# Optimization experiments

Hardware: AMD Instinct MI355X
Metric: run time of the kernel (lower is better)

The kernel has to match this reference:

```python
import math
import jax, jax.numpy as jnp
import numpy as np

V, D, H, L, F, S, B = 32000, 768, 12, 6, 3072, 2048, 4
DK = D // H


def setup_inputs() -> dict:
    key = jax.random.key(0)
    ks = jax.random.split(key, 16)
    sc = 0.02
    n = jax.random.normal
    inp = {
        "input_ids": jax.random.randint(ks[0], (B, S), 0, V, dtype=jnp.int64)
        if jax.config.jax_enable_x64 else jax.random.randint(ks[0], (B, S), 0, V, dtype=jnp.int32),
        "emb": n(ks[1], (V, D), jnp.float32) * sc,
        "Wq": n(ks[2], (L, D, D), jnp.float32) * sc, "bq": jnp.zeros((L, D), jnp.float32),
        "Wk": n(ks[3], (L, D, D), jnp.float32) * sc, "bk": jnp.zeros((L, D), jnp.float32),
        "Wv": n(ks[4], (L, D, D), jnp.float32) * sc, "bv": jnp.zeros((L, D), jnp.float32),
        "Wo": n(ks[5], (L, D, D), jnp.float32) * sc, "bo": jnp.zeros((L, D), jnp.float32),
        "W1": n(ks[6], (L, D, F), jnp.float32) * sc, "b1": jnp.zeros((L, F), jnp.float32),
        "W2": n(ks[7], (L, F, D), jnp.float32) * sc, "b2": jnp.zeros((L, D), jnp.float32),
        "gamma": jnp.ones((L, D), jnp.float32), "beta": jnp.zeros((L, D), jnp.float32),
    }
    return inp


def _pos_encoding(seq_len, d):
    pos = jnp.arange(seq_len, dtype=jnp.float32)[:, None]                  # [S,1]
    div = jnp.exp(jnp.arange(0, d, 2, dtype=jnp.float32) * (-math.log(10000.0) / d))
    ang = pos * div                                                        # [S,D/2]
    return jnp.stack([jnp.sin(ang), jnp.cos(ang)], axis=-1).reshape(seq_len, d)


def _layernorm(x, g, b, eps=1e-5):
    mu = x.mean(-1, keepdims=True)
    var = ((x - mu) ** 2).mean(-1, keepdims=True)
    return (x - mu) * jax.lax.rsqrt(var + eps) * g + b


def _forward(input_ids, emb, Wq, bq, Wk, bk, Wv, bv, Wo, bo, W1, b1, W2, b2, gamma, beta):
    mask = (input_ids != 1)[:, None, None, :]                              # [B,1,1,S]
    x = emb[input_ids] + _pos_encoding(input_ids.shape[1], emb.shape[1])   # [B,S,D]

    def layer(x, p):
        wq, bq_, wk, bk_, wv, bv_, wo, bo_, w1, b1_, w2, b2_, g, bt = p
        def heads(h):  # [B,S,D] -> [B,H,S,DK]
            return h.reshape(B, S, H, DK).transpose(0, 2, 1, 3)
        q = heads(x @ wq + bq_)
        k = heads(x @ wk + bk_)
        v = heads(x @ wv + bv_)
        scores = jnp.einsum("bhqd,bhkd->bhqk", q, k) / math.sqrt(DK)
        scores = jnp.where(mask, scores, -1e9)
        attn = jax.nn.softmax(scores, axis=-1)
        o = jnp.einsum("bhqk,bhkd->bhqd", attn, v)
        o = o.transpose(0, 2, 1, 3).reshape(B, S, D) @ wo + bo_
        x1 = _layernorm(x + o, g, bt)
        ff = jax.nn.relu(x1 @ w1 + b1_) @ w2 + b2_
        return _layernorm(x1 + ff, g, bt), None  # same norm params reused (as in source)

    x, _ = jax.lax.scan(layer, x, (Wq, bq, Wk, bk, Wv, bv, Wo, bo, W1, b1, W2, b2, gamma, beta))
    return x.mean(axis=1)                                                  # [B,D]


def reference(input_ids, emb, Wq, bq, Wk, bk, Wv, bv, Wo, bo, W1, b1, W2, b2, gamma, beta):
    return _forward(input_ids, emb, Wq, bq, Wk, bk, Wv, bv, Wo, bo, W1, b1, W2, b2, gamma, beta)
```

## Files before the change

### kernel.cpp

```cpp
#include <hip/hip_runtime.h>
#include <hip/hip_bf16.h>
#include <math.h>

typedef unsigned short u16;
typedef unsigned long long u64;
using bf16x8 = __attribute__((ext_vector_type(8))) short;
using f32x4  = __attribute__((ext_vector_type(4))) float;

static constexpr int kD = 768;
static constexpr int kH = 12;
static constexpr int kL = 6;
static constexpr int kF = 3072;
static constexpr int kS = 2048;
static constexpr int kB = 4;
static constexpr int kQW = 2304;
static constexpr int kNT = kB * kS;

static constexpr float kQScale = 0.18033688011112043f;

__device__ __forceinline__ u16 f2bf(float f) {
    return __bfloat16_as_ushort(__float2bfloat16(f));
}
__device__ __forceinline__ float b2f(u16 u) {
    return __uint_as_float((unsigned)u << 16);
}
__device__ __forceinline__ unsigned cvtpk(float a, float b) {
    unsigned d;
    asm volatile("v_cvt_pk_bf16_f32 %0, %1, %2" : "=v"(d) : "v"(a), "v"(b));
    return d;
}
__device__ __forceinline__ float exp2fast(float x) {
#if __has_builtin(__builtin_amdgcn_exp2f)
    return __builtin_amdgcn_exp2f(x);
#else
    return __expf(x * 0.6931471805599453f);
#endif
}

__device__ __forceinline__ void gload16(const void* g, void* l) {
    auto gp = reinterpret_cast<const __attribute__((address_space(1))) unsigned int*>(
        reinterpret_cast<uintptr_t>(g));
    auto lp = reinterpret_cast<__attribute__((address_space(3))) unsigned int*>(
        reinterpret_cast<uintptr_t>(l));
    __builtin_amdgcn_global_load_lds(gp, lp, 16, 0, 0);
}

__global__ __launch_bounds__(256) void embed_pe(
    const int* __restrict__ ids, const float* __restrict__ emb,
    u16* __restrict__ xbf)
{
    const int t = blockIdx.x;
    const int s = t & (kS - 1);
    const int id = ids[t];
#pragma unroll
    for (int j = 0; j < 3; ++j) {
        const int d = threadIdx.x + (j << 8);
        const float i2 = (float)((d >> 1) << 1);
        const float dv = __expf(i2 * (-9.210340371976184f / 768.f));
        const float ang = (float)s * dv;
        const float pe = (d & 1) ? cosf(ang) : sinf(ang);
        xbf[(size_t)t * kD + d] = f2bf(emb[(size_t)id * kD + d] + pe);
    }
}

__global__ __launch_bounds__(256) void embed_pe_f32(
    const int* __restrict__ ids, const float* __restrict__ emb,
    float* __restrict__ x)
{
    const int t = blockIdx.x;
    const int s = t & (kS - 1);
    const int id = ids[t];
#pragma unroll
    for (int j = 0; j < 3; ++j) {
        const int d = threadIdx.x + (j << 8);
        const float i2 = (float)((d >> 1) << 1);
        const float dv = __expf(i2 * (-9.210340371976184f / 768.f));
        const float ang = (float)s * dv;
        const float pe = (d & 1) ? cosf(ang) : sinf(ang);
        x[(size_t)t * kD + d] = emb[(size_t)id * kD + d] + pe;
    }
}

__global__ __launch_bounds__(64) void mk_maskbits(const int* __restrict__ ids,
                                                  u64* __restrict__ mbits)
{
    const int w = blockIdx.x;
    const int lane = threadIdx.x;
    const u64 m = __ballot(ids[(size_t)w * 64 + lane] != 1);
    if (lane == 0) mbits[w] = m;
}

__global__ __launch_bounds__(256) void bias_build(
    const float* __restrict__ bq, const float* __restrict__ bk,
    const float* __restrict__ bv, const float* __restrict__ bo,
    const float* __restrict__ b1, const float* __restrict__ b2,
    float* __restrict__ ba)
{
    const int i = blockIdx.x * 256 + threadIdx.x;
    if (i >= 6 * 6912) return;
    const int l = i / 6912, p = i % 6912;
    float v;
    if      (p < 768)  v = bq[l * 768 + p] * kQScale;
    else if (p < 1536) v = bk[l * 768 + p - 768];
    else if (p < 2304) v = bv[l * 768 + p - 1536];
    else if (p < 3072) v = bo[l * 768 + p - 2304];
    else if (p < 6144) v = b1[(size_t)l * 3072 + p - 3072];
    else               v = b2[l * 768 + p - 6144];
    ba[i] = v;
}

static constexpr size_t OFF_WO = (size_t)2304 * 768;
static constexpr size_t OFF_W1 = OFF_WO + (size_t)768 * 768;
static constexpr size_t OFF_W2 = OFF_W1 + (size_t)3072 * 768;
static constexpr size_t WARENA_E = OFF_W2 + (size_t)768 * 3072;

__global__ __launch_bounds__(256) void cvt_all(
    const float* __restrict__ Wq, const float* __restrict__ Wk,
    const float* __restrict__ Wv, const float* __restrict__ Wo,
    const float* __restrict__ W1, const float* __restrict__ W2,
    u16* __restrict__ wa)
{
    __shared__ float T[64][68];
    const int t = blockIdx.x;
    const float* S; u16* Dp; int Nsrc, Kdst, srow0, scol0; float sc = 1.f;
    if (t < 432) {
        const int ni = t % 36, ki = t / 36;
        const int ng = ni * 64;
        const int sel = ng / 768;
        scol0 = ng % 768; srow0 = ki * 64;
        S = (sel == 0) ? Wq : (sel == 1) ? Wk : Wv;
        if (sel == 0) sc = kQScale;
        Nsrc = 768; Kdst = 768;
        Dp = wa + (size_t)ng * 768 + srow0;
    } else if (t < 576) {
        const int tt = t - 432; const int ni = tt % 12, ki = tt / 12;
        scol0 = ni * 64; srow0 = ki * 64;
        S = Wo; Nsrc = 768; Kdst = 768;
        Dp = wa + OFF_WO + (size_t)(ni * 64) * 768 + srow0;
    } else if (t < 1152) {
        const int tt = t - 576; const int ni = tt % 48, ki = tt / 48;
        scol0 = ni * 64; srow0 = ki * 64;
        S = W1; Nsrc = 3072; Kdst = 768;
        Dp = wa + OFF_W1 + (size_t)(ni * 64) * 768 + srow0;
    } else {
        const int tt = t - 1152; const int ni = tt % 12, ki = tt / 12;
        scol0 = ni * 64; srow0 = ki * 64;
        S = W2; Nsrc = 768; Kdst = 3072;
        Dp = wa + OFF_W2 + (size_t)(ni * 64) * 3072 + srow0;
    }
    const int tid = threadIdx.x;
#pragma unroll
    for (int i = 0; i < 4; ++i) {
        const int idx = tid + (i << 8);
        const int kr = idx >> 4;
        const int nc = (idx & 15) << 2;
        const float4 v = *(const float4*)(S + (size_t)(srow0 + kr) * Nsrc + scol0 + nc);
        T[kr][nc] = v.x; T[kr][nc + 1] = v.y; T[kr][nc + 2] = v.z; T[kr][nc + 3] = v.w;
    }
    __syncthreads();
#pragma unroll
    for (int i = 0; i < 4; ++i) {
        const int idx = tid + (i << 8);
        const int nr = idx >> 4;
        const int kc = (idx & 15) << 2;
        ushort4 o;
        o.x = f2bf(T[kc][nr] * sc);     o.y = f2bf(T[kc + 1][nr] * sc);
        o.z = f2bf(T[kc + 2][nr] * sc); o.w = f2bf(T[kc + 3][nr] * sc);
        *(ushort4*)(Dp + (size_t)nr * Kdst + kc) = o;
    }
}

__global__ __launch_bounds__(256) void gemm_bf16(
    const u16* __restrict__ A, const u16* __restrict__ Bt,
    const float* __restrict__ bias, void* __restrict__ Cv,
    u16* __restrict__ vTp, int M, int N, int K, int mode)
{
    __shared__ u16 As[2][4096];
    __shared__ u16 Bs[2][4096];
    const int tid = threadIdx.x;
    const int l = tid & 63;
    const int lo = l & 15, hi = l >> 4;
    const int w = tid >> 6, wr = w >> 1, wc = w & 1;

    int brow = blockIdx.x, bcol = blockIdx.y;
    const int gx = gridDim.x;
    if ((gx & 7) == 0) {
        const int id = blockIdx.y * gx + blockIdx.x;
        const int xcd = id & 7, idx = id >> 3;
        const int rpx = gx >> 3;
        brow = xcd * rpx + (idx % rpx);
        bcol = idx / rpx;
    }
    const size_t row0 = (size_t)brow * 128;
    const size_t col0 = (size_t)bcol * 128;

    const int c0 = tid, c1 = tid + 256;
    const int r0 = c0 >> 2, g0 = (c0 & 3) ^ ((r0 >> 1) & 3);
    const int r1 = c1 >> 2, g1 = (c1 & 3) ^ ((r1 >> 1) & 3);
    const u16* a0 = A  + (row0 + r0) * K + g0 * 8;
    const u16* a1 = A  + (row0 + r1) * K + g1 * 8;
    const u16* b0 = Bt + (col0 + r0) * K + g0 * 8;
    const u16* b1 = Bt + (col0 + r1) * K + g1 * 8;

    f32x4 acc[4][4];
#pragma unroll
    for (int i = 0; i < 4; ++i)
#pragma unroll
        for (int j = 0; j < 4; ++j)
#pragma unroll
            for (int r = 0; r < 4; ++r) acc[i][j][r] = 0.f;

    int aoff[4], boff[4];
#pragma unroll
    for (int i = 0; i < 4; ++i) {
        const int ra = wr * 64 + i * 16 + lo;
        aoff[i] = ra * 32 + ((hi ^ ((ra >> 1) & 3)) << 3);
        const int rb = wc * 64 + i * 16 + lo;
        boff[i] = rb * 32 + ((hi ^ ((rb >> 1) & 3)) << 3);
    }

    const int NT = K >> 5;
    gload16(a0, As[0] + c0 * 8);
    gload16(a1, As[0] + c1 * 8);
    gload16(b0, Bs[0] + c0 * 8);
    gload16(b1, Bs[0] + c1 * 8);

    int cur = 0;
    for (int t = 0; t < NT; ++t) {
        if (t + 1 < NT) {
            const int k0 = (t + 1) << 5;
            const int nb = cur ^ 1;
            gload16(a0 + k0, As[nb] + c0 * 8);
            gload16(a1 + k0, As[nb] + c1 * 8);
            gload16(b0 + k0, Bs[nb] + c0 * 8);
            gload16(b1 + k0, Bs[nb] + c1 * 8);
            asm volatile("s_waitcnt vmcnt(4)" ::: "memory");
        } else {
            asm volatile("s_waitcnt vmcnt(0)" ::: "memory");
        }
        __builtin_amdgcn_s_barrier();
        bf16x8 af[4], bfr[4];
#pragma unroll
        for (int i = 0; i < 4; ++i) af[i]  = *(const bf16x8*)&As[cur][aoff[i]];
#pragma unroll
        for (int j = 0; j < 4; ++j) bfr[j] = *(const bf16x8*)&Bs[cur][boff[j]];
#pragma unroll
        for (int i = 0; i < 4; ++i)
#pragma unroll
            for (int j = 0; j < 4; ++j)
                acc[i][j] = __builtin_amdgcn_mfma_f32_16x16x32_bf16(
                    af[i], bfr[j], acc[i][j], 0, 0, 0);
        asm volatile("s_waitcnt lgkmcnt(0)" ::: "memory");
        __builtin_amdgcn_sched_barrier(0);
        __builtin_amdgcn_s_barrier();
        cur ^= 1;
    }

    const bool vmode = (mode == 3) && (col0 >= 1536);
    if (vmode) {
#pragma unroll
        for (int i = 0; i < 4; ++i) {
            const size_t rbase = row0 + wr * 64 + i * 16 + hi * 4;
            const size_t tb = (rbase >> 6) * 64;
            const int k0 = (int)(rbase & 63);
            const int pos = (((k0 >> 2) & 3) << 3) + (((k0 >> 4) & 1) << 2)
                          + ((k0 >> 5) << 5);
#pragma unroll
            for (int j = 0; j < 4; ++j) {
                const size_t c = col0 + wc * 64 + j * 16 + lo;
                const float bs = bias[c];
                const size_t d = c - 1536;
                ushort4 o;
                o.x = f2bf(acc[i][j][0] + bs);
                o.y = f2bf(acc[i][j][1] + bs);
                o.z = f2bf(acc[i][j][2] + bs);
                o.w = f2bf(acc[i][j][3] + bs);
                *(ushort4*)(vTp + d * (size_t)M + tb + pos) = o;
            }
        }
        return;
    }

#pragma unroll
    for (int i = 0; i < 4; ++i) {
        const size_t rbase = row0 + wr * 64 + i * 16 + hi * 4;
#pragma unroll
        for (int j = 0; j < 4; ++j) {
            const size_t c = col0 + wc * 64 + j * 16 + lo;
            const float bs = bias[c];
#pragma unroll
            for (int r = 0; r < 4; ++r) {
                float v = acc[i][j][r] + bs;
                if (mode == 2) v = fmaxf(v, 0.f);
                ((u16*)Cv)[(rbase + r) * (size_t)N + c] = f2bf(v);
            }
        }
    }
}

__global__ __launch_bounds__(256) void attn_mfma(
    const u16* __restrict__ QKV, const u16* __restrict__ vT,
    const u64* __restrict__ mbits, u16* __restrict__ O)
{
    __shared__ u16 Ks[2][4096];
    __shared__ u16 Vs[2][4096];

    const int tid = threadIdx.x, l = tid & 63, w = tid >> 6;
    const int lo = l & 15, hi = l >> 4;
    const int h = blockIdx.y, b = blockIdx.z;
    const int q0 = blockIdx.x << 6;

    bf16x8 qf0, qf1;
    {
        const u16* qp = QKV + ((size_t)(b * kS + q0 + w * 16 + lo)) * kQW
                            + h * 64 + hi * 8;
        qf0 = *(const bf16x8*)qp;
        qf1 = *(const bf16x8*)(qp + 32);
    }

    const int ga = tid, gb = tid + 256;
    const int rwA = ga >> 3, sxA = ga & 7, EA = sxA ^ (rwA & 7);
    const int rwB = gb >> 3, sxB = gb & 7, EB = sxB ^ (rwB & 7);
    const u16* Kbase = QKV + (size_t)(b * kS) * kQW + 768 + h * 64;
    const u16* Vbase = vT + (size_t)(h * 64) * kNT + b * kS;

    f32x4 accO[4];
#pragma unroll
    for (int n = 0; n < 4; ++n)
#pragma unroll
        for (int r = 0; r < 4; ++r) accO[n][r] = 0.f;
    float m = -3.0e38f, lsum = 0.f;

    const int ksw = (lo & 7) << 3;
    constexpr int NTt = kS / 64;

    gload16(Kbase + (size_t)rwA * kQW + EA * 8, Ks[0] + ga * 8);
    gload16(Kbase + (size_t)rwB * kQW + EB * 8, Ks[0] + gb * 8);
    gload16(Vbase + (size_t)rwA * kNT + EA * 8, Vs[0] + ga * 8);
    gload16(Vbase + (size_t)rwB * kNT + EB * 8, Vs[0] + gb * 8);

    int cur = 0;
    for (int kt = 0; kt < NTt; ++kt) {
        asm volatile("s_waitcnt vmcnt(0)" ::: "memory");
        __syncthreads();

        if (kt + 1 < NTt) {
            const size_t kof = (size_t)((kt + 1) << 6) * kQW;
            const size_t vof = (size_t)((kt + 1) << 6);
            u16* kd = Ks[cur ^ 1];
            u16* vd = Vs[cur ^ 1];
            gload16(Kbase + kof + (size_t)rwA * kQW + EA * 8, kd + ga * 8);
            gload16(Kbase + kof + (size_t)rwB * kQW + EB * 8, kd + gb * 8);
            gload16(Vbase + (size_t)rwA * kNT + vof + EA * 8, vd + ga * 8);
            gload16(Vbase + (size_t)rwB * kNT + vof + EB * 8, vd + gb * 8);
        }

        f32x4 st[4];
        __builtin_amdgcn_s_setprio(1);
#pragma unroll
        for (int j = 0; j < 4; ++j) {
#pragma unroll
            for (int r = 0; r < 4; ++r) st[j][r] = 0.f;
            const int kb2 = (j * 16 + lo) * 64;
            const bf16x8 k0 = *(const bf16x8*)&Ks[cur][kb2 + ((hi * 8)      ^ ksw)];
            const bf16x8 k1 = *(const bf16x8*)&Ks[cur][kb2 + ((hi * 8 + 32) ^ ksw)];
            st[j] = __builtin_amdgcn_mfma_f32_16x16x32_bf16(k0, qf0, st[j], 0, 0, 0);
            st[j] = __builtin_amdgcn_mfma_f32_16x16x32_bf16(k1, qf1, st[j], 0, 0, 0);
        }
        __builtin_amdgcn_s_setprio(0);

        float rmax = st[0][0];
#pragma unroll
        for (int j = 0; j < 4; ++j)
#pragma unroll
            for (int r = 0; r < 4; ++r) rmax = fmaxf(rmax, st[j][r]);
        rmax = fmaxf(rmax, __shfl_xor(rmax, 16));
        rmax = fmaxf(rmax, __shfl_xor(rmax, 32));

        const bool skip = __all(rmax <= m + 11.0f);
        if (!skip) {
            const float mn = fmaxf(m, rmax);
            const float corr = exp2fast(m - mn);
            m = mn;
            lsum *= corr;
            float c2[4];
#pragma unroll
            for (int r = 0; r < 4; ++r) c2[r] = __shfl(corr, hi * 4 + r);
#pragma unroll
            for (int n = 0; n < 4; ++n)
#pragma unroll
                for (int r = 0; r < 4; ++r) accO[n][r] *= c2[r];
        }

#pragma unroll
        for (int j = 0; j < 4; ++j)
#pragma unroll
            for (int r = 0; r < 4; ++r) st[j][r] = exp2fast(st[j][r] - m);

        const u64 mb = mbits[b * 32 + kt];
        if (mb != ~0ull) {
#pragma unroll
            for (int j = 0; j < 4; ++j)
#pragma unroll
                for (int r = 0; r < 4; ++r)
                    if (!((mb >> (j * 16 + hi * 4 + r)) & 1)) st[j][r] = 0.f;
        }

        float ts = 0.f;
#pragma unroll
        for (int j = 0; j < 4; ++j)
#pragma unroll
            for (int r = 0; r < 4; ++r) ts += st[j][r];
        ts += __shfl_xor(ts, 16);
        ts += __shfl_xor(ts, 32);
        lsum += ts;

        union PU { unsigned u[4]; bf16x8 v; } p0, p1;
        p0.u[0] = cvtpk(st[0][0], st[0][1]); p0.u[1] = cvtpk(st[0][2], st[0][3]);
        p0.u[2] = cvtpk(st[1][0], st[1][1]); p0.u[3] = cvtpk(st[1][2], st[1][3]);
        p1.u[0] = cvtpk(st[2][0], st[2][1]); p1.u[1] = cvtpk(st[2][2], st[2][3]);
        p1.u[2] = cvtpk(st[3][0], st[3][1]); p1.u[3] = cvtpk(st[3][2], st[3][3]);

        __builtin_amdgcn_s_setprio(1);
#pragma unroll
        for (int n = 0; n < 4; ++n) {
            const int vb2 = (n * 16 + lo) * 64;
            const bf16x8 v0 = *(const bf16x8*)&Vs[cur][vb2 + ((hi * 8)      ^ ksw)];
            const bf16x8 v1 = *(const bf16x8*)&Vs[cur][vb2 + ((hi * 8 + 32) ^ ksw)];
            accO[n] = __builtin_amdgcn_mfma_f32_16x16x32_bf16(p0.v, v0, accO[n], 0, 0, 0);
            accO[n] = __builtin_amdgcn_mfma_f32_16x16x32_bf16(p1.v, v1, accO[n], 0, 0, 0);
        }
        __builtin_amdgcn_s_setprio(0);
        cur ^= 1;
    }

    float linv[4];
#pragma unroll
    for (int r = 0; r < 4; ++r) linv[r] = 1.f / __shfl(lsum, hi * 4 + r);
#pragma unroll
    for (int n = 0; n < 4; ++n)
#pragma unroll
        for (int r = 0; r < 4; ++r)
            O[((size_t)(b * kS + q0 + w * 16 + hi * 4 + r)) * kD
              + h * 64 + n * 16 + lo] = f2bf(accO[n][r] * linv[r]);
}

__global__ __launch_bounds__(256) void add_ln_bf(
    const u16* __restrict__ a, const u16* __restrict__ r,
    const float* __restrict__ g, const float* __restrict__ bt,
    u16* __restrict__ out)
{
    const int lane = threadIdx.x & 63;
    const size_t row = (size_t)blockIdx.x * 4 + (threadIdx.x >> 6);
    const ushort4* a4 = (const ushort4*)(a + row * kD);
    const ushort4* r4 = (const ushort4*)(r + row * kD);
    float v[3][4];
    float s = 0.f;
#pragma unroll
    for (int j = 0; j < 3; ++j) {
        const ushort4 av = a4[j * 64 + lane];
        const ushort4 rv = r4[j * 64 + lane];
        v[j][0] = b2f(av.x) + b2f(rv.x);
        v[j][1] = b2f(av.y) + b2f(rv.y);
        v[j][2] = b2f(av.z) + b2f(rv.z);
        v[j][3] = b2f(av.w) + b2f(rv.w);
        s += v[j][0] + v[j][1] + v[j][2] + v[j][3];
    }
#pragma unroll
    for (int off = 32; off; off >>= 1) s += __shfl_xor(s, off);
    const float mu = s * (1.f / 768.f);
    float vs = 0.f;
#pragma unroll
    for (int j = 0; j < 3; ++j)
#pragma unroll
        for (int e = 0; e < 4; ++e) {
            const float t0 = v[j][e] - mu;
            vs = fmaf(t0, t0, vs);
        }
#pragma unroll
    for (int off = 32; off; off >>= 1) vs += __shfl_xor(vs, off);
    const float rstd = rsqrtf(vs * (1.f / 768.f) + 1e-5f);
    const float4* g4 = (const float4*)g;
    const float4* b4 = (const float4*)bt;
#pragma unroll
    for (int j = 0; j < 3; ++j) {
        const float4 gv = g4[j * 64 + lane];
        const float4 bv = b4[j * 64 + lane];
        ushort4 o;
        o.x = f2bf((v[j][0] - mu) * rstd * gv.x + bv.x);
        o.y = f2bf((v[j][1] - mu) * rstd * gv.y + bv.y);
        o.z = f2bf((v[j][2] - mu) * rstd * gv.z + bv.z);
        o.w = f2bf((v[j][3] - mu) * rstd * gv.w + bv.w);
        ((ushort4*)(out + row * kD))[j * 64 + lane] = o;
    }
}

__global__ __launch_bounds__(192) void mean_part_bf(
    const u16* __restrict__ x, float* __restrict__ mred)
{
    const int c = blockIdx.x, b = blockIdx.y;
    const int d = threadIdx.x * 4;
    const u16* base = x + ((size_t)b * kS + c * 32) * kD + d;
    float s0 = 0.f, s1 = 0.f, s2 = 0.f, s3 = 0.f;
#pragma unroll 8
    for (int t = 0; t < 32; ++t) {
        const ushort4 u = *(const ushort4*)(base + (size_t)t * kD);
        s0 += b2f(u.x); s1 += b2f(u.y); s2 += b2f(u.z); s3 += b2f(u.w);
    }
    float4 o; o.x = s0; o.y = s1; o.z = s2; o.w = s3;
    *(float4*)(mred + ((size_t)b * 64 + c) * kD + d) = o;
}

__global__ __launch_bounds__(256) void mean_fin(
    const float* __restrict__ mred, float* __restrict__ out)
{
    const int d = blockIdx.x * 256 + threadIdx.x;
    const int b = blockIdx.y;
    float s = 0.f;
#pragma unroll
    for (int c = 0; c < 64; ++c) s += mred[((size_t)b * 64 + c) * kD + d];
    out[b * kD + d] = s * (1.f / 2048.f);
}

__global__ __launch_bounds__(256) void add_ln_f32(
    const float* __restrict__ a, const float* __restrict__ r,
    const float* __restrict__ g, const float* __restrict__ bt,
    float* __restrict__ out)
{
    const int lane = threadIdx.x & 63;
    const size_t row = (size_t)blockIdx.x * 4 + (threadIdx.x >> 6);
    const float4* a4 = (const float4*)(a + row * kD);
    const float4* r4 = (const float4*)(r + row * kD);
    float4 v[3];
    float s = 0.f;
#pragma unroll
    for (int j = 0; j < 3; ++j) {
        const float4 av = a4[j * 64 + lane];
        const float4 rv = r4[j * 64 + lane];
        v[j].x = av.x + rv.x; v[j].y = av.y + rv.y;
        v[j].z = av.z + rv.z; v[j].w = av.w + rv.w;
        s += v[j].x + v[j].y + v[j].z + v[j].w;
    }
#pragma unroll
    for (int off = 32; off; off >>= 1) s += __shfl_xor(s, off);
    const float mu = s * (1.f / 768.f);
    float vs = 0.f;
#pragma unroll
    for (int j = 0; j < 3; ++j) {
        float t0 = v[j].x - mu, t1 = v[j].y - mu, t2 = v[j].z - mu, t3 = v[j].w - mu;
        vs = fmaf(t0, t0, fmaf(t1, t1, fmaf(t2, t2, fmaf(t3, t3, vs))));
    }
#pragma unroll
    for (int off = 32; off; off >>= 1) vs += __shfl_xor(vs, off);
    const float rstd = rsqrtf(vs * (1.f / 768.f) + 1e-5f);
    const float4* g4 = (const float4*)g;
    const float4* b4 = (const float4*)bt;
#pragma unroll
    for (int j = 0; j < 3; ++j) {
        const float4 gv = g4[j * 64 + lane];
        const float4 bv = b4[j * 64 + lane];
        float4 o;
        o.x = (v[j].x - mu) * rstd * gv.x + bv.x;
        o.y = (v[j].y - mu) * rstd * gv.y + bv.y;
        o.z = (v[j].z - mu) * rstd * gv.z + bv.z;
        o.w = (v[j].w - mu) * rstd * gv.w + bv.w;
        ((float4*)(out + row * kD))[j * 64 + lane] = o;
    }
}

__global__ __launch_bounds__(256) void mean_s(
    const float* __restrict__ x, float* __restrict__ out)
{
    const int d = blockIdx.x * 256 + threadIdx.x;
    const int b = blockIdx.y;
    float s = 0.f;
    for (int t = 0; t < kS; ++t) s += x[((size_t)b * kS + t) * kD + d];
    out[b * kD + d] = s * (1.f / 2048.f);
}

__global__ __launch_bounds__(256) void gemm_f32(
    const float* __restrict__ A, const float* __restrict__ W,
    const float* __restrict__ bias, float* __restrict__ C,
    int M, int N, int K, int relu)
{
    __shared__ float As[16][68];
    __shared__ float Bs[16][68];
    const int tid = threadIdx.x;
    const int row0 = blockIdx.x << 6;
    const int col0 = blockIdx.y << 6;
    const int tx = tid & 15, ty = tid >> 4;
    const int ar = tid >> 2;
    const int ak = (tid & 3) << 2;
    const int bk = tid >> 4;
    const int bc = (tid & 15) << 2;
    float acc[4][4] = {};
    const float* Ap = A + (size_t)(row0 + ar) * K + ak;
    const float* Wp = W + (size_t)bk * N + col0 + bc;
    for (int k0 = 0; k0 < K; k0 += 16) {
        const float4 a4 = *(const float4*)(Ap + k0);
        const float4 b4 = *(const float4*)(Wp + (size_t)k0 * N);
        __syncthreads();
        As[ak + 0][ar] = a4.x; As[ak + 1][ar] = a4.y;
        As[ak + 2][ar] = a4.z; As[ak + 3][ar] = a4.w;
        *(float4*)&Bs[bk][bc] = b4;
        __syncthreads();
#pragma unroll
        for (int kk = 0; kk < 16; ++kk) {
            const float4 av = *(const float4*)&As[kk][ty << 2];
            const float4 bv = *(const float4*)&Bs[kk][tx << 2];
            const float aa[4] = {av.x, av.y, av.z, av.w};
            const float bb[4] = {bv.x, bv.y, bv.z, bv.w};
#pragma unroll
            for (int i = 0; i < 4; ++i)
#pragma unroll
                for (int j = 0; j < 4; ++j)
                    acc[i][j] = fmaf(aa[i], bb[j], acc[i][j]);
        }
    }
#pragma unroll
    for (int i = 0; i < 4; ++i) {
        const int row = row0 + (ty << 2) + i;
#pragma unroll
        for (int j = 0; j < 4; ++j) {
            const int col = col0 + (tx << 2) + j;
            float v = acc[i][j] + bias[col];
            if (relu) v = fmaxf(v, 0.f);
            C[(size_t)row * N + col] = v;
        }
    }
}

__global__ __launch_bounds__(256) void attn_fused(
    const float* __restrict__ Q, const float* __restrict__ Km,
    const float* __restrict__ Vm, const int* __restrict__ ids,
    float* __restrict__ O)
{
    __shared__ float Ksf[64 * 64];
    __shared__ float Vtf[64 * 64];
    __shared__ float Qs[16][64];
    __shared__ float Psf[4][4][64];
    const int tid = threadIdx.x;
    const int w = tid >> 6;
    const int lane = tid & 63;
    const int h = blockIdx.y, b = blockIdx.z;
    const int qrow0 = blockIdx.x << 4;
    {
        const int r = tid >> 4;
        const int c4 = tid & 15;
        const float4 q4 = *(const float4*)(
            Q + ((size_t)(b * kS + qrow0 + r)) * kD + h * 64 + (c4 << 2));
        Qs[r][(c4 << 2) + 0] = q4.x * 0.125f;
        Qs[r][(c4 << 2) + 1] = q4.y * 0.125f;
        Qs[r][(c4 << 2) + 2] = q4.z * 0.125f;
        Qs[r][(c4 << 2) + 3] = q4.w * 0.125f;
    }
    float m[4], lsum[4], o[4];
#pragma unroll
    for (int r = 0; r < 4; ++r) { m[r] = -3.0e38f; lsum[r] = 0.f; o[r] = 0.f; }
    for (int kt = 0; kt < kS / 64; ++kt) {
        __syncthreads();
#pragma unroll
        for (int i = 0; i < 4; ++i) {
            const int lin = tid + (i << 8);
            const int row = lin >> 4;
            const int s4 = lin & 15;
            const size_t gro = ((size_t)(b * kS + (kt << 6) + row)) * kD + h * 64 + (s4 << 2);
            const float4 k4 = *(const float4*)(Km + gro);
            ((float4*)Ksf)[(row << 4) + (s4 ^ (row & 7))] = k4;
            const float4 v4 = *(const float4*)(Vm + gro);
            const int ksl = row >> 2, ke = row & 3;
            const int d0 = s4 << 2;
            Vtf[(d0 + 0) * 64 + ((ksl ^ ((d0 + 0) & 7)) << 2) + ke] = v4.x;
            Vtf[(d0 + 1) * 64 + ((ksl ^ ((d0 + 1) & 7)) << 2) + ke] = v4.y;
            Vtf[(d0 + 2) * 64 + ((ksl ^ ((d0 + 2) & 7)) << 2) + ke] = v4.z;
            Vtf[(d0 + 3) * 64 + ((ksl ^ ((d0 + 3) & 7)) << 2) + ke] = v4.w;
        }
        __syncthreads();
        const bool masked = (ids[(size_t)b * kS + (kt << 6) + lane] == 1);
        float scr[4] = {0.f, 0.f, 0.f, 0.f};
#pragma unroll
        for (int i16 = 0; i16 < 16; ++i16) {
            const float4 kv = ((const float4*)Ksf)[(lane << 4) + (i16 ^ (lane & 7))];
#pragma unroll
            for (int r = 0; r < 4; ++r) {
                const float4 qv = *(const float4*)&Qs[(w << 2) + r][i16 << 2];
                scr[r] = fmaf(kv.x, qv.x, fmaf(kv.y, qv.y,
                          fmaf(kv.z, qv.z, fmaf(kv.w, qv.w, scr[r]))));
            }
        }
#pragma unroll
        for (int r = 0; r < 4; ++r) {
            float sm = masked ? -3.0e38f : scr[r];
#pragma unroll
            for (int off = 32; off; off >>= 1) sm = fmaxf(sm, __shfl_xor(sm, off));
            const float mn = fmaxf(m[r], sm);
            const float cr = __expf(m[r] - mn);
            const float pv = masked ? 0.f : __expf(scr[r] - mn);
            float ps = pv;
#pragma unroll
            for (int off = 32; off; off >>= 1) ps += __shfl_xor(ps, off);
            lsum[r] = lsum[r] * cr + ps;
            o[r] *= cr;
            m[r] = mn;
            Psf[w][r][lane] = pv;
        }
#pragma unroll
        for (int i16 = 0; i16 < 16; ++i16) {
            const float4 vv = ((const float4*)Vtf)[(lane << 4) + (i16 ^ (lane & 7))];
#pragma unroll
            for (int r = 0; r < 4; ++r) {
                const float4 pv = *(const float4*)&Psf[w][r][i16 << 2];
                o[r] = fmaf(pv.x, vv.x, fmaf(pv.y, vv.y,
                        fmaf(pv.z, vv.z, fmaf(pv.w, vv.w, o[r]))));
            }
        }
    }
#pragma unroll
    for (int r = 0; r < 4; ++r)
        O[((size_t)(b * kS + qrow0 + (w << 2) + r)) * kD + h * 64 + lane] =
            o[r] / lsum[r];
}

extern "C" void kernel_launch(void* const* d_in, const int* in_sizes, int n_in,
                              void* d_out, int out_size, void* d_ws, size_t ws_size,
                              hipStream_t stream)
{
    const int*   ids   = (const int*)  d_in[0];
    const float* emb   = (const float*)d_in[1];
    const float* Wq    = (const float*)d_in[2];
    const float* bq    = (const float*)d_in[3];
    const float* Wk    = (const float*)d_in[4];
    const float* bk    = (const float*)d_in[5];
    const float* Wv    = (const float*)d_in[6];
    const float* bv    = (const float*)d_in[7];
    const float* Wo    = (const float*)d_in[8];
    const float* bo    = (const float*)d_in[9];
    const float* W1    = (const float*)d_in[10];
    const float* b1    = (const float*)d_in[11];
    const float* W2    = (const float*)d_in[12];
    const float* b2    = (const float*)d_in[13];
    const float* gamma = (const float*)d_in[14];
    const float* beta  = (const float*)d_in[15];
    float* out = (float*)d_out;

    const size_t BUFE = (size_t)kB * kS * kD;
    const size_t WDD  = (size_t)kD * kD;
    const size_t WDF  = (size_t)kD * kF;
    const size_t HIDE = (size_t)kB * kS * kF;
    const int NTOK = kB * kS;

    const size_t NEED = BUFE * 2 * 4
                      + HIDE * 2
                      + WARENA_E * 2
                      + (size_t)6 * 6912 * 4
                      + 128 * 8
                      + (size_t)kB * 64 * kD * 4;

    if (ws_size >= NEED) {
        u16*   xb  = (u16*)d_ws;
        u16*   x1b = xb + BUFE;
        u16*   ao  = x1b + BUFE;
        u16*   ob  = ao + BUFE;
        u16*   sc  = ob + BUFE;
        u16*   vtb = sc + (size_t)NTOK * kQW;
        u16*   wa  = sc + HIDE;
        float* ba  = (float*)(wa + WARENA_E);
        u64*   mbt = (u64*)(ba + 6 * 6912);
        float* mrd = (float*)(mbt + 128);

        embed_pe<<<NTOK, 256, 0, stream>>>(ids, emb, xb);
        mk_maskbits<<<kB * kS / 64, 64, 0, stream>>>(ids, mbt);
        bias_build<<<(6 * 6912 + 255) / 256, 256, 0, stream>>>(
            bq, bk, bv, bo, b1, b2, ba);

        for (int l = 0; l < kL; ++l) {
            const size_t oDD = (size_t)l * WDD;
            const size_t oDF = (size_t)l * WDF;
            const float* bl = ba + (size_t)l * 6912;
            const float* gl  = gamma + (size_t)l * kD;
            const float* btl = beta  + (size_t)l * kD;

            cvt_all<<<1728, 256, 0, stream>>>(
                Wq + oDD, Wk + oDD, Wv + oDD, Wo + oDD, W1 + oDF, W2 + oDF, wa);

            gemm_bf16<<<dim3(64, 18), 256, 0, stream>>>(
                xb, wa, bl, sc, vtb, NTOK, kQW, kD, 3);

            attn_mfma<<<dim3(kS / 64, kH, kB), 256, 0, stream>>>(
                sc, vtb, mbt, ao);

            gemm_bf16<<<dim3(64, 6), 256, 0, stream>>>(
                ao, wa + OFF_WO, bl + 2304, ob, nullptr, NTOK, kD, kD, 1);

            add_ln_bf<<<NTOK / 4, 256, 0, stream>>>(xb, ob, gl, btl, x1b);

            gemm_bf16<<<dim3(64, 24), 256, 0, stream>>>(
                x1b, wa + OFF_W1, bl + 3072, sc, nullptr, NTOK, kF, kD, 2);
            gemm_bf16<<<dim3(64, 6), 256, 0, stream>>>(
                sc, wa + OFF_W2, bl + 6144, ob, nullptr, NTOK, kD, kF, 1);

            add_ln_bf<<<NTOK / 4, 256, 0, stream>>>(x1b, ob, gl, btl, xb);
        }

        mean_part_bf<<<dim3(64, kB), 192, 0, stream>>>(xb, mrd);
        mean_fin<<<dim3(kD / 256, kB), 256, 0, stream>>>(mrd, out);
        return;
    }

    if (ws_size < 5 * BUFE * sizeof(float)) return;
    float* xb = (float*)d_ws;
    float* kb = xb + BUFE;
    float* qb = kb + BUFE;
    float* vb = qb + BUFE;
    float* obf = vb + BUFE;
    float* hb = qb;

    embed_pe_f32<<<NTOK, 256, 0, stream>>>(ids, emb, xb);
    for (int l = 0; l < kL; ++l) {
        const size_t oDD = (size_t)l * WDD;
        const size_t oDF = (size_t)l * WDF;
        gemm_f32<<<dim3(NTOK / 64, kD / 64), 256, 0, stream>>>(
            xb, Wq + oDD, bq + (size_t)l * kD, qb, NTOK, kD, kD, 0);
        gemm_f32<<<dim3(NTOK / 64, kD / 64), 256, 0, stream>>>(
            xb, Wk + oDD, bk + (size_t)l * kD, kb, NTOK, kD, kD, 0);
        gemm_f32<<<dim3(NTOK / 64, kD / 64), 256, 0, stream>>>(
            xb, Wv + oDD, bv + (size_t)l * kD, vb, NTOK, kD, kD, 0);
        attn_fused<<<dim3(kS / 16, kH, kB), 256, 0, stream>>>(qb, kb, vb, ids, obf);
        gemm_f32<<<dim3(NTOK / 64, kD / 64), 256, 0, stream>>>(
            obf, Wo + oDD, bo + (size_t)l * kD, qb, NTOK, kD, kD, 0);
        add_ln_f32<<<NTOK / 4, 256, 0, stream>>>(xb, qb,
            gamma + (size_t)l * kD, beta + (size_t)l * kD, kb);
        for (int c = 0; c < 2; ++c) {
            const size_t ro = (size_t)c * 4096;
            gemm_f32<<<dim3(4096 / 64, kF / 64), 256, 0, stream>>>(
                kb + ro * kD, W1 + oDF, b1 + (size_t)l * kF, hb, 4096, kF, kD, 1);
            gemm_f32<<<dim3(4096 / 64, kD / 64), 256, 0, stream>>>(
                hb, W2 + oDF, b2 + (size_t)l * kD, obf + ro * kD, 4096, kD, kF, 0);
        }
        add_ln_f32<<<NTOK / 4, 256, 0, stream>>>(kb, obf,
            gamma + (size_t)l * kD, beta + (size_t)l * kD, xb);
    }
    mean_s<<<dim3(kD / 256, kB), 256, 0, stream>>>(xb, out);
}
```

Measured before the change: 1.662 ms.

## Add 256x256 triple-buffered GEMM and 128-query attention blocks with XCD remap

Adds a 512-thread GEMM kernel with 256x256 output tiles and a three-stage LDS pipeline, used for the QKV and FFN-up projections. Larger tiles raise data reuse per loaded byte, and the extra stage lets global loads run further ahead of the MFMA work. The attention kernel now runs 512 threads covering 128 queries per block, with a flattened block index remapped across the XCDs so each K/V tile is shared by more queries. Costs include much higher register and LDS use per block, fewer blocks in the grid (288 and 384) which may leave CUs idle, and the old V-transpose path is removed from the 128x128 GEMM.

```diff
diff --git a/kernel.cpp b/kernel.cpp
--- a/kernel.cpp
+++ b/kernel.cpp
@@ -170,6 +170,142 @@
     }
 }
 
+__global__ __launch_bounds__(512, 1) void gemm256(
+    const u16* __restrict__ A, const u16* __restrict__ Bt,
+    const float* __restrict__ bias, void* __restrict__ Cv,
+    u16* __restrict__ vTp, int M, int N, int K, int mode)
+{
+    __shared__ u16 As[3][8192];
+    __shared__ u16 Bs[3][8192];
+    const int tid = threadIdx.x;
+    const int l = tid & 63;
+    const int lo = l & 15, hi = l >> 4;
+    const int w = tid >> 6, wr = w >> 2, wc = w & 3;
+
+    int brow = blockIdx.x, bcol = blockIdx.y;
+    const int gx = gridDim.x;
+    if ((gx & 7) == 0) {
+        const int id = blockIdx.y * gx + blockIdx.x;
+        const int xcd = id & 7, idx = id >> 3;
+        const int rpx = gx >> 3;
+        brow = xcd * rpx + (idx % rpx);
+        bcol = idx / rpx;
+    }
+    const size_t row0 = (size_t)brow * 256;
+    const size_t col0 = (size_t)bcol * 256;
+
+    const int c0 = tid, c1 = tid + 512;
+    const int r0 = c0 >> 2, g0 = (c0 & 3) ^ ((r0 >> 1) & 3);
+    const int r1 = c1 >> 2, g1 = (c1 & 3) ^ ((r1 >> 1) & 3);
+    const u16* a0 = A  + (row0 + r0) * K + g0 * 8;
+    const u16* a1 = A  + (row0 + r1) * K + g1 * 8;
+    const u16* b0 = Bt + (col0 + r0) * K + g0 * 8;
+    const u16* b1 = Bt + (col0 + r1) * K + g1 * 8;
+
+    f32x4 acc[8][4];
+#pragma unroll
+    for (int i = 0; i < 8; ++i)
+#pragma unroll
+        for (int j = 0; j < 4; ++j)
+#pragma unroll
+            for (int r = 0; r < 4; ++r) acc[i][j][r] = 0.f;
+
+    int aoff[8], boff[4];
+#pragma unroll
+    for (int i = 0; i < 8; ++i) {
+        const int ra = wr * 128 + i * 16 + lo;
+        aoff[i] = ra * 32 + ((hi ^ ((ra >> 1) & 3)) << 3);
+    }
+#pragma unroll
+    for (int j = 0; j < 4; ++j) {
+        const int rb = wc * 64 + j * 16 + lo;
+        boff[j] = rb * 32 + ((hi ^ ((rb >> 1) & 3)) << 3);
+    }
+
+    const int NT = K >> 5;
+#pragma unroll
+    for (int t = 0; t < 2; ++t) {
+        const int k0 = t << 5;
+        gload16(a0 + k0, As[t] + c0 * 8);
+        gload16(a1 + k0, As[t] + c1 * 8);
+        gload16(b0 + k0, Bs[t] + c0 * 8);
+        gload16(b1 + k0, Bs[t] + c1 * 8);
+    }
+
+    int cur = 0;
+    for (int t = 0; t < NT; ++t) {
+        if (t + 1 < NT) {
+            asm volatile("s_waitcnt vmcnt(8)" ::: "memory");
+        } else {
+            asm volatile("s_waitcnt vmcnt(0)" ::: "memory");
+        }
+        __builtin_amdgcn_s_barrier();
+        if (t + 2 < NT) {
+            const int k0 = (t + 2) << 5;
+            const int nb = (cur + 2 >= 3) ? cur - 1 : cur + 2;
+            gload16(a0 + k0, As[nb] + c0 * 8);
+            gload16(a1 + k0, As[nb] + c1 * 8);
+            gload16(b0 + k0, Bs[nb] + c0 * 8);
+            gload16(b1 + k0, Bs[nb] + c1 * 8);
+        }
+        bf16x8 af[8], bfr[4];
+#pragma unroll
+        for (int i = 0; i < 8; ++i) af[i]  = *(const bf16x8*)&As[cur][aoff[i]];
+#pragma unroll
+        for (int j = 0; j < 4; ++j) bfr[j] = *(const bf16x8*)&Bs[cur][boff[j]];
+        __builtin_amdgcn_s_setprio(1);
+#pragma unroll
+        for (int i = 0; i < 8; ++i)
+#pragma unroll
+            for (int j = 0; j < 4; ++j)
+                acc[i][j] = __builtin_amdgcn_mfma_f32_16x16x32_bf16(
+                    af[i], bfr[j], acc[i][j], 0, 0, 0);
+        __builtin_amdgcn_s_setprio(0);
+        cur = (cur + 1 == 3) ? 0 : cur + 1;
+    }
+
+    const bool vmode = (mode == 3) && (col0 >= 1536);
+    if (vmode) {
+#pragma unroll
+        for (int i = 0; i < 8; ++i) {
+            const size_t rbase = row0 + wr * 128 + i * 16 + hi * 4;
+            const size_t tb = (rbase >> 6) * 64;
+            const int k0 = (int)(rbase & 63);
+            const int pos = (((k0 >> 2) & 3) << 3) + (((k0 >> 4) & 1) << 2)
+                          + ((k0 >> 5) << 5);
+#pragma unroll
+            for (int j = 0; j < 4; ++j) {
+                const size_t c = col0 + wc * 64 + j * 16 + lo;
+                const float bs = bias[c];
+                const size_t d = c - 1536;
+                ushort4 o;
+                o.x = f2bf(acc[i][j][0] + bs);
+                o.y = f2bf(acc[i][j][1] + bs);
+                o.z = f2bf(acc[i][j][2] + bs);
+                o.w = f2bf(acc[i][j][3] + bs);
+                *(ushort4*)(vTp + d * (size_t)M + tb + pos) = o;
+            }
+        }
+        return;
+    }
+
+#pragma unroll
+    for (int i = 0; i < 8; ++i) {
+        const size_t rbase = row0 + wr * 128 + i * 16 + hi * 4;
+#pragma unroll
+        for (int j = 0; j < 4; ++j) {
+            const size_t c = col0 + wc * 64 + j * 16 + lo;
+            const float bs = bias[c];
+#pragma unroll
+            for (int r = 0; r < 4; ++r) {
+                float v = acc[i][j][r] + bs;
+                if (mode == 2) v = fmaxf(v, 0.f);
+                ((u16*)Cv)[(rbase + r) * (size_t)N + c] = f2bf(v);
+            }
+        }
+    }
+}
+
 __global__ __launch_bounds__(256) void gemm_bf16(
     const u16* __restrict__ A, const u16* __restrict__ Bt,
     const float* __restrict__ bias, void* __restrict__ Cv,
@@ -256,31 +392,6 @@
         cur ^= 1;
     }
 
-    const bool vmode = (mode == 3) && (col0 >= 1536);
-    if (vmode) {
-#pragma unroll
-        for (int i = 0; i < 4; ++i) {
-            const size_t rbase = row0 + wr * 64 + i * 16 + hi * 4;
-            const size_t tb = (rbase >> 6) * 64;
-            const int k0 = (int)(rbase & 63);
-            const int pos = (((k0 >> 2) & 3) << 3) + (((k0 >> 4) & 1) << 2)
-                          + ((k0 >> 5) << 5);
-#pragma unroll
-            for (int j = 0; j < 4; ++j) {
-                const size_t c = col0 + wc * 64 + j * 16 + lo;
-                const float bs = bias[c];
-                const size_t d = c - 1536;
-                ushort4 o;
-                o.x = f2bf(acc[i][j][0] + bs);
-                o.y = f2bf(acc[i][j][1] + bs);
-                o.z = f2bf(acc[i][j][2] + bs);
-                o.w = f2bf(acc[i][j][3] + bs);
-                *(ushort4*)(vTp + d * (size_t)M + tb + pos) = o;
-            }
-        }
-        return;
-    }
-
 #pragma unroll
     for (int i = 0; i < 4; ++i) {
         const size_t rbase = row0 + wr * 64 + i * 16 + hi * 4;
@@ -298,7 +409,7 @@
     }
 }
 
-__global__ __launch_bounds__(256) void attn_mfma(
+__global__ __launch_bounds__(512) void attn_mfma(
     const u16* __restrict__ QKV, const u16* __restrict__ vT,
     const u64* __restrict__ mbits, u16* __restrict__ O)
 {
@@ -307,8 +418,13 @@
 
     const int tid = threadIdx.x, l = tid & 63, w = tid >> 6;
     const int lo = l & 15, hi = l >> 4;
-    const int h = blockIdx.y, b = blockIdx.z;
-    const int q0 = blockIdx.x << 6;
+
+    const int flat = blockIdx.x + 16 * (blockIdx.y + 12 * blockIdx.z);
+    const int nf = (flat & 7) * 96 + (flat >> 3);
+    const int qi = nf & 15;
+    const int h  = (nf >> 4) % 12;
+    const int b  = nf / 192;
+    const int q0 = qi << 7;
 
     bf16x8 qf0, qf1;
     {
@@ -318,9 +434,7 @@
         qf1 = *(const bf16x8*)(qp + 32);
     }
 
-    const int ga = tid, gb = tid + 256;
-    const int rwA = ga >> 3, sxA = ga & 7, EA = sxA ^ (rwA & 7);
-    const int rwB = gb >> 3, sxB = gb & 7, EB = sxB ^ (rwB & 7);
+    const int rw = tid >> 3, sx = tid & 7, E = sx ^ (rw & 7);
     const u16* Kbase = QKV + (size_t)(b * kS) * kQW + 768 + h * 64;
     const u16* Vbase = vT + (size_t)(h * 64) * kNT + b * kS;
 
@@ -334,10 +448,8 @@
     const int ksw = (lo & 7) << 3;
     constexpr int NTt = kS / 64;
 
-    gload16(Kbase + (size_t)rwA * kQW + EA * 8, Ks[0] + ga * 8);
-    gload16(Kbase + (size_t)rwB * kQW + EB * 8, Ks[0] + gb * 8);
-    gload16(Vbase + (size_t)rwA * kNT + EA * 8, Vs[0] + ga * 8);
-    gload16(Vbase + (size_t)rwB * kNT + EB * 8, Vs[0] + gb * 8);
+    gload16(Kbase + (size_t)rw * kQW + E * 8, Ks[0] + tid * 8);
+    gload16(Vbase + (size_t)rw * kNT + E * 8, Vs[0] + tid * 8);
 
     int cur = 0;
     for (int kt = 0; kt < NTt; ++kt) {
@@ -347,12 +459,8 @@
         if (kt + 1 < NTt) {
             const size_t kof = (size_t)((kt + 1) << 6) * kQW;
             const size_t vof = (size_t)((kt + 1) << 6);
-            u16* kd = Ks[cur ^ 1];
-            u16* vd = Vs[cur ^ 1];
-            gload16(Kbase + kof + (size_t)rwA * kQW + EA * 8, kd + ga * 8);
-            gload16(Kbase + kof + (size_t)rwB * kQW + EB * 8, kd + gb * 8);
-            gload16(Vbase + (size_t)rwA * kNT + vof + EA * 8, vd + ga * 8);
-            gload16(Vbase + (size_t)rwB * kNT + vof + EB * 8, vd + gb * 8);
+            gload16(Kbase + kof + (size_t)rw * kQW + E * 8, Ks[cur ^ 1] + tid * 8);
+            gload16(Vbase + (size_t)rw * kNT + vof + E * 8, Vs[cur ^ 1] + tid * 8);
         }
 
         f32x4 st[4];
@@ -783,10 +891,10 @@
             cvt_all<<<1728, 256, 0, stream>>>(
                 Wq + oDD, Wk + oDD, Wv + oDD, Wo + oDD, W1 + oDF, W2 + oDF, wa);
 
-            gemm_bf16<<<dim3(64, 18), 256, 0, stream>>>(
+            gemm256<<<dim3(32, 9), 512, 0, stream>>>(
                 xb, wa, bl, sc, vtb, NTOK, kQW, kD, 3);
 
-            attn_mfma<<<dim3(kS / 64, kH, kB), 256, 0, stream>>>(
+            attn_mfma<<<dim3(kS / 128, kH, kB), 512, 0, stream>>>(
                 sc, vtb, mbt, ao);
 
             gemm_bf16<<<dim3(64, 6), 256, 0, stream>>>(
@@ -794,7 +902,7 @@
 
             add_ln_bf<<<NTOK / 4, 256, 0, stream>>>(xb, ob, gl, btl, x1b);
 
-            gemm_bf16<<<dim3(64, 24), 256, 0, stream>>>(
+            gemm256<<<dim3(32, 12), 512, 0, stream>>>(
                 x1b, wa + OFF_W1, bl + 3072, sc, nullptr, NTOK, kF, kD, 2);
             gemm_bf16<<<dim3(64, 6), 256, 0, stream>>>(
                 sc, wa + OFF_W2, bl + 6144, ob, nullptr, NTOK, kD, kF, 1);
```

After: 1.612 ms. 1.03x faster.
